# Kernel optimization log

Hardware: AMD Instinct MI355X
Metric: run time of the kernel (lower is better)

Reference implementation:

```python
import jax, jax.numpy as jnp
import numpy as np

B, C, H, W = 4, 128, 64, 64
THITA = 1e-4


def conv1x1(x, w, b):
    # 1x1 conv + bias + ReLU; x:[B,Cin,H,W], w:[Cout,Cin], b:[Cout]
    return jax.nn.relu(jnp.einsum('bihw,oi->bohw', x, w) + b[None, :, None, None])


_CONV_SPECS = [
    ('neighbor', 2 * C, 4),
    ('pro_key', C, C), ('pro_val', C, C),
    ('lat_key', C, C), ('lat_val', C, C),
    ('tmp1', C, 2 * C),
    ('now1', C, 2),
    ('now_key', C, C), ('now_val', C, C),
    ('q', C, C), ('k', C, C), ('v', C, C),
]


def setup_inputs() -> dict:
    key = jax.random.key(0)
    ks = jax.random.split(key, 1 + 2 * len(_CONV_SPECS))
    inp = {'event': jax.random.normal(ks[0], (B, 6, H, W), dtype=jnp.float32)}
    i = 1
    for name, o, c in _CONV_SPECS:
        s = 1.0 / np.sqrt(c)
        inp['w_' + name] = jax.random.uniform(ks[i], (o, c), minval=-s, maxval=s, dtype=jnp.float32)
        inp['b_' + name] = jax.random.uniform(ks[i + 1], (o,), minval=-s, maxval=s, dtype=jnp.float32)
        i += 2
    return inp


def reference(event, w_neighbor, b_neighbor, w_pro_key, b_pro_key, w_pro_val, b_pro_val,
              w_lat_key, b_lat_key, w_lat_val, b_lat_val, w_tmp1, b_tmp1,
              w_now1, b_now1, w_now_key, b_now_key, w_now_val, b_now_val,
              w_q, b_q, w_k, b_k, w_v, b_v):
    pro, now, lat = event[:, 0:2], event[:, 2:4], event[:, 4:6]
    neigh = conv1x1(jnp.concatenate([pro, lat], axis=1), w_neighbor, b_neighbor)  # [B,2C,H,W]
    pro_key = conv1x1(neigh[:, :C], w_pro_key, b_pro_key)
    pro_val = conv1x1(neigh[:, C:], w_pro_val, b_pro_val)
    lat_key = conv1x1(neigh[:, :C], w_lat_key, b_lat_key)
    lat_val = conv1x1(neigh[:, C:], w_lat_val, b_lat_val)
    # NOTE: source applies conv_tmp1 (shared weights) to both key and val paths
    key_n = conv1x1(jnp.concatenate([pro_key, lat_key], axis=1), w_tmp1, b_tmp1)
    val_n = conv1x1(jnp.concatenate([pro_val, lat_val], axis=1), w_tmp1, b_tmp1)
    now_f = conv1x1(now, w_now1, b_now1)
    now_key = conv1x1(now_f, w_now_key, b_now_key)
    now_val = conv1x1(now_f, w_now_val, b_now_val)
    N = H * W
    q = conv1x1(key_n, w_q, b_q).reshape(B, C, N)          # proj_query pre-permute
    k = conv1x1(now_key, w_k, b_k).reshape(B, C, N)        # [B,C,N]
    attn = jax.nn.softmax(jnp.einsum('bcn,bcm->bnm', q, k), axis=-1)  # [B,N,N]
    v = conv1x1(val_n, w_v, b_v).reshape(B, C, N)
    out = jnp.einsum('bcm,bnm->bcn', v, attn).reshape(B, C, H, W)
    return THITA * out + now_val
```

## Files before the change

kernel.cpp:

```cpp
#include <hip/hip_runtime.h>

#define B_ 4
#define C_ 128
#define N_ 4096
#define LOG2E 1.44269504088896340736f

typedef __attribute__((ext_vector_type(8))) __bf16 bf16x8;
typedef __attribute__((ext_vector_type(16))) float f32x16;

#define SWZ(n) (((n) & 15) << 4)

__device__ __forceinline__ unsigned short cvb(float x) {
    return __builtin_bit_cast(unsigned short, (__bf16)x);
}
__device__ __forceinline__ unsigned pk2(float lo, float hi) {
    return (unsigned)cvb(lo) | ((unsigned)cvb(hi) << 16);
}
__device__ __forceinline__ float bfu(unsigned short u) {
    return __builtin_bit_cast(float, (unsigned)u << 16);
}
__device__ __forceinline__ float fexp2(float x) {
#if __has_builtin(__builtin_amdgcn_exp2f)
    return __builtin_amdgcn_exp2f(x);
#else
    float r;
    asm("v_exp_f32 %0, %1" : "=v"(r) : "v"(x));
    return r;
#endif
}
__device__ inline void gload_lds16(const void* g, void* l) {
    __builtin_amdgcn_global_load_lds(
        (const __attribute__((address_space(1))) unsigned int*)g,
        (__attribute__((address_space(3))) unsigned int*)l, 16, 0, 0);
}
__device__ __forceinline__ void plswapf(float& a, float& b) {
    asm volatile("v_permlane32_swap_b32 %0, %1" : "+v"(a), "+v"(b));
}
__device__ __forceinline__ void plswapu(unsigned& a, unsigned& b) {
    asm volatile("v_permlane32_swap_b32 %0, %1" : "+v"(a), "+v"(b));
}

__global__ __launch_bounds__(256) void k_wcvt(
        const float* pk, const float* lk, const float* pv, const float* lv,
        const float* t1, const float* nk, const float* nv,
        const float* q, const float* k, const float* v,
        const float* bpk, const float* blk, const float* bpv, const float* blv,
        const float* bnk, const float* bnv,
        unsigned short* Wk, unsigned short* Wv, unsigned short* Wt1,
        unsigned short* Wnow, unsigned short* Wq, unsigned short* Wkk,
        unsigned short* Wvv, float* bck, float* bcv, float* bcn) {
    int i = blockIdx.x * 256 + threadIdx.x;
    if (i < 22528) {
        int c = i;
        const float *s0, *s1 = nullptr;
        unsigned short* dst;
        int ks;
        if      (c < 4096)  { dst = Wk;   ks = 3; s0 = pk; s1 = lk; }
        else if (c < 8192)  { dst = Wv;   ks = 3; s0 = pv; s1 = lv; c -= 4096; }
        else if (c < 12288) { dst = Wt1;  ks = 4; s0 = t1;          c -= 8192; }
        else if (c < 16384) { dst = Wnow; ks = 3; s0 = nk; s1 = nv; c -= 12288; }
        else if (c < 18432) { dst = Wq;   ks = 3; s0 = q;           c -= 16384; }
        else if (c < 20480) { dst = Wkk;  ks = 3; s0 = k;           c -= 18432; }
        else                { dst = Wvv;  ks = 3; s0 = v;           c -= 20480; }
        int K = 16 << ks;
        int lane = c & 63, tile = c >> 6;
        int mt = tile >> ks, kt = tile & ((1 << ks) - 1);
        int row = mt * 32 + (lane & 31);
        int col = kt * 16 + (lane >> 5) * 8;
        const float* src = (s1 && row >= 128) ? (s1 + (size_t)(row - 128) * K + col)
                                              : (s0 + (size_t)row * K + col);
        unsigned short ov[8];
        #pragma unroll
        for (int j = 0; j < 8; ++j) ov[j] = cvb(src[j]);
        *(uint4*)(dst + (size_t)c * 8) = *(const uint4*)ov;
    }
    else if (i < 22784) { int j = i - 22528; bck[j] = j < 128 ? bpk[j] : blk[j - 128]; }
    else if (i < 23040) { int j = i - 22784; bcv[j] = j < 128 ? bpv[j] : blv[j - 128]; }
    else if (i < 23296) { int j = i - 23040; bcn[j] = j < 128 ? bnk[j] : bnv[j - 128]; }
}

template<int KSTEPS, int ROWB>
__device__ __forceinline__ f32x16 gtile(const char* Ab, int aChBase,
        const unsigned short* Wf, int mchunk, int nl, int h) {
    f32x16 acc;
    #pragma unroll
    for (int r = 0; r < 16; ++r) acc[r] = 0.f;
    const char* arow = Ab + nl * ROWB;
    const unsigned short* wb = Wf + ((size_t)mchunk * KSTEPS) * 512 + (nl + 32 * h) * 8;
    #pragma unroll
    for (int kk = 0; kk < KSTEPS; ++kk) {
        bf16x8 a = *(const bf16x8*)(arow + ((aChBase + kk * 32 + h * 16) ^ SWZ(nl)));
        bf16x8 wf = *(const bf16x8*)(wb + kk * 512);
        acc = __builtin_amdgcn_mfma_f32_32x32x16_bf16(a, wf, acc, 0, 0, 0);
    }
    return acc;
}

__device__ __forceinline__ void epi_lds(char* dst, int rowB, f32x16 acc,
        const float* bias, int m0, int nl, int h) {
    int m = m0 + nl;
    float bs = bias[m];
    #pragma unroll
    for (int r = 0; r < 16; ++r) {
        int n = (r & 3) + 8 * (r >> 2) + 4 * h;
        *(unsigned short*)(dst + n * rowB + ((m * 2) ^ SWZ(n))) =
            cvb(fmaxf(acc[r] + bs, 0.f));
    }
}

__device__ __forceinline__ void epi_nc(unsigned short* Y, f32x16 acc,
        const float* bias, float scale, int m0, int n0g, int b, int nl, int h) {
    int m = m0 + nl;
    float bs = bias[m];
    #pragma unroll
    for (int r = 0; r < 16; ++r) {
        int n = (r & 3) + 8 * (r >> 2) + 4 * h;
        Y[((size_t)b * N_ + n0g + n) * C_ + m] = cvb(fmaxf(acc[r] + bs, 0.f) * scale);
    }
}

__device__ __forceinline__ void epi_cn_b16(unsigned short* Y, f32x16 acc,
        const float* bias, int m0, int n0g, int b, int nl, int h) {
    int m = m0 + nl;
    float bs = bias[m];
    #pragma unroll
    for (int r2 = 0; r2 < 4; ++r2) {
        int nn = 8 * r2 + 4 * h;
        uint2 o;
        o.x = pk2(fmaxf(acc[4*r2+0] + bs, 0.f), fmaxf(acc[4*r2+1] + bs, 0.f));
        o.y = pk2(fmaxf(acc[4*r2+2] + bs, 0.f), fmaxf(acc[4*r2+3] + bs, 0.f));
        *(uint2*)(Y + ((size_t)b * C_ + m) * N_ + n0g + nn) = o;
    }
}

__global__ __launch_bounds__(256) void k_chain(
        const float* __restrict__ ev, const float* __restrict__ w_nb,
        const float* __restrict__ b_nb, const float* __restrict__ w_n1,
        const float* __restrict__ b_n1,
        const unsigned short* __restrict__ Wk, const unsigned short* __restrict__ Wv,
        const unsigned short* __restrict__ Wt1, const unsigned short* __restrict__ Wnow,
        const unsigned short* __restrict__ Wq, const unsigned short* __restrict__ Wkk,
        const unsigned short* __restrict__ Wvv,
        const float* __restrict__ bck, const float* __restrict__ bcv,
        const float* __restrict__ bt1, const float* __restrict__ bcn,
        const float* __restrict__ bq, const float* __restrict__ bk,
        const float* __restrict__ bv,
        unsigned short* __restrict__ Qt, unsigned short* __restrict__ Kb,
        unsigned short* __restrict__ Vb, unsigned short* __restrict__ NowVb) {
    __shared__ char lds[49152];
    char* NEIGH = lds;
    char* KCAT  = lds + 16384;
    char* VCAT  = lds + 32768;
    char* KEYN  = lds;
    char* VALN  = lds + 8192;
    char* NOWF  = lds + 16384;
    char* NOWK  = lds + 24576;

    const int t = threadIdx.x, lane = t & 63, w = t >> 6;
    const int nl = lane & 31, h = lane >> 5;
    const int b = blockIdx.y;
    const int n0g = blockIdx.x * 32;
    const int m0 = w * 32;
    const int mc = w;

    uint2 nf[4];
    {
        int n = t & 31, grp = t >> 5;
        const float* evb = ev + (size_t)b * 6 * N_ + n0g + n;
        float e0 = evb[0], e1 = evb[N_], e4 = evb[4*N_], e5 = evb[5*N_];
        float e2 = evb[2*N_], e3 = evb[3*N_];
        int och0 = grp * 32;
        #pragma unroll
        for (int i = 0; i < 32; i += 4) {
            float r_[4];
            #pragma unroll
            for (int j = 0; j < 4; ++j) {
                int o = och0 + i + j;
                float4 w4 = *(const float4*)(w_nb + o * 4);
                r_[j] = fmaxf(b_nb[o] + w4.x*e0 + w4.y*e1 + w4.z*e4 + w4.w*e5, 0.f);
            }
            uint2 val; val.x = pk2(r_[0], r_[1]); val.y = pk2(r_[2], r_[3]);
            *(uint2*)(NEIGH + n * 512 + (((och0 + i) * 2) ^ SWZ(n))) = val;
        }
        int o0 = grp * 16;
        #pragma unroll
        for (int i2 = 0; i2 < 4; ++i2) {
            float r_[4];
            #pragma unroll
            for (int j = 0; j < 4; ++j) {
                int o = o0 + i2 * 4 + j;
                float2 w2 = *(const float2*)(w_n1 + o * 2);
                r_[j] = fmaxf(b_n1[o] + w2.x*e2 + w2.y*e3, 0.f);
            }
            nf[i2].x = pk2(r_[0], r_[1]); nf[i2].y = pk2(r_[2], r_[3]);
        }
    }
    __syncthreads();

    {
        f32x16 a0 = gtile<8, 512>(NEIGH, 0,   Wk, mc,     nl, h);
        f32x16 a1 = gtile<8, 512>(NEIGH, 0,   Wk, mc + 4, nl, h);
        f32x16 a2 = gtile<8, 512>(NEIGH, 256, Wv, mc,     nl, h);
        f32x16 a3 = gtile<8, 512>(NEIGH, 256, Wv, mc + 4, nl, h);
        epi_lds(KCAT, 512, a0, bck, m0,       nl, h);
        epi_lds(KCAT, 512, a1, bck, m0 + 128, nl, h);
        epi_lds(VCAT, 512, a2, bcv, m0,       nl, h);
        epi_lds(VCAT, 512, a3, bcv, m0 + 128, nl, h);
    }
    __syncthreads();

    {
        f32x16 a0 = gtile<16, 512>(KCAT, 0, Wt1, mc, nl, h);
        f32x16 a1 = gtile<16, 512>(VCAT, 0, Wt1, mc, nl, h);
        epi_lds(KEYN, 256, a0, bt1, m0, nl, h);
        epi_lds(VALN, 256, a1, bt1, m0, nl, h);
    }
    __syncthreads();

    {
        int n = t & 31, grp = t >> 5;
        int o0 = grp * 16;
        #pragma unroll
        for (int i2 = 0; i2 < 4; ++i2)
            *(uint2*)(NOWF + n * 256 + (((o0 + i2 * 4) * 2) ^ SWZ(n))) = nf[i2];
    }
    __syncthreads();

    {
        f32x16 a0 = gtile<8, 256>(NOWF, 0, Wnow, mc,     nl, h);
        f32x16 a1 = gtile<8, 256>(NOWF, 0, Wnow, mc + 4, nl, h);
        epi_lds(NOWK, 256, a0, bcn, m0, nl, h);
        epi_cn_b16(NowVb, a1, bcn + 128, m0, n0g, b, nl, h);
    }
    __syncthreads();

    {
        f32x16 aq = gtile<8, 256>(KEYN, 0, Wq,  mc, nl, h);
        f32x16 ak = gtile<8, 256>(NOWK, 0, Wkk, mc, nl, h);
        f32x16 av = gtile<8, 256>(VALN, 0, Wvv, mc, nl, h);
        epi_nc(Qt, aq, bq, LOG2E, m0, n0g, b, nl, h);
        epi_nc(Kb, ak, bk, 1.0f,  m0, n0g, b, nl, h);
        epi_cn_b16(Vb, av, bv, m0, n0g, b, nl, h);
    }
}

#define SPLIT 4
#define CHUNK 32

__global__ __launch_bounds__(128) void k_flashp(
        const unsigned short* __restrict__ Qt, const unsigned short* __restrict__ Kt,
        const unsigned short* __restrict__ Vb,
        unsigned short* __restrict__ Opb, float* __restrict__ ML) {
    __shared__ char stg[2][16384];
    const int t = threadIdx.x;
    const int lane = t & 63;
    const int nh = t >> 6;
    const int h = lane >> 5, nl = lane & 31;
    const int i_ = blockIdx.x;
    const int mpb = (i_ & 7) + 8 * ((i_ >> 3) & 1);
    const int ntile = i_ >> 4;
    const int mp = mpb >> 2, b = mpb & 3;
    const int n0 = ntile * 64 + nh * 32;
    const size_t bo = (size_t)b * N_ * C_;

    bf16x8 qf[8];
    {
        const char* qb = (const char*)(Qt + bo);
        #pragma unroll
        for (int kk = 0; kk < 8; ++kk)
            qf[kk] = *(const bf16x8*)(qb + (size_t)(n0 + nl) * 256 + kk*32 + h*16);
    }

    const char* ktb = (const char*)(Kt + bo);
    const char* vbb = (const char*)(Vb + bo);

    f32x16 oa[4];
    #pragma unroll
    for (int ss = 0; ss < 4; ++ss)
        #pragma unroll
        for (int r = 0; r < 16; ++r) oa[ss][r] = 0.f;
    float m_run = -1e30f, l_run = 0.f;

    const int swzK = (nl & 15) << 4;
    const int swzV = ((nl >> 1) & 7) << 4;

    auto stage = [&](int tile, int ph) {
        char* base = stg[ph];
        if (nh == 0) {
            const char* src = ktb + (size_t)tile * 8192;
            #pragma unroll
            for (int ii = 0; ii < 8; ++ii) {
                int L = ii*1024 + lane*16;
                int T = L ^ (((L >> 8) & 15) << 4);
                gload_lds16(src + T, base + ii*1024);
            }
        } else {
            const char* src = vbb + (size_t)tile * 64;
            #pragma unroll
            for (int ii = 0; ii < 8; ++ii) {
                int L = ii*1024 + lane*16;
                int T = L ^ (((L >> 7) & 7) << 4);
                int c = T >> 6, inner = T & 63;
                gload_lds16(src + (size_t)c * (N_*2) + inner, base + 8192 + ii*1024);
            }
        }
    };

    const int tb = mp * CHUNK;
    stage(tb, 0);
    stage(tb + 1, 1);

    for (int it = 0; it < CHUNK; ++it) {
        int ph = it & 1;
        if (it < CHUNK - 1) asm volatile("s_waitcnt vmcnt(8)" ::: "memory");
        else                asm volatile("s_waitcnt vmcnt(0)" ::: "memory");
        __builtin_amdgcn_s_barrier();
        __builtin_amdgcn_sched_barrier(0);
        const char* kb = stg[ph];
        const char* vb = kb + 8192;

        f32x16 s;
        #pragma unroll
        for (int r = 0; r < 16; ++r) s[r] = 0.f;
        __builtin_amdgcn_s_setprio(1);
        #pragma unroll
        for (int kk = 0; kk < 8; ++kk) {
            int y = nl*256 + kk*32 + h*16;
            bf16x8 a = *(const bf16x8*)(kb + (y ^ swzK));
            s = __builtin_amdgcn_mfma_f32_32x32x16_bf16(a, qf[kk], s, 0, 0, 0);
        }
        __builtin_amdgcn_s_setprio(0);

        float tm = fmaxf(fmaxf(fmaxf(s[0], s[1]), fmaxf(s[2], s[3])),
                         fmaxf(fmaxf(s[4], s[5]), fmaxf(s[6], s[7])));
        float tm2 = fmaxf(fmaxf(fmaxf(s[8], s[9]), fmaxf(s[10], s[11])),
                          fmaxf(fmaxf(s[12], s[13]), fmaxf(s[14], s[15])));
        tm = fmaxf(tm, tm2);
        { float x = tm, y = tm; plswapf(x, y); tm = fmaxf(x, y); }
        if (!__all(tm <= m_run + 8.f)) {
            float mn = fmaxf(m_run, tm);
            float sc = fexp2(m_run - mn);
            m_run = mn;
            l_run *= sc;
            #pragma unroll
            for (int ss = 0; ss < 4; ++ss)
                #pragma unroll
                for (int r = 0; r < 16; ++r) oa[ss][r] *= sc;
        }
        float p[16];
        float ls = 0.f;
        #pragma unroll
        for (int r = 0; r < 16; ++r) { p[r] = fexp2(s[r] - m_run); ls += p[r]; }
        { float x = ls, y = ls; plswapf(x, y); ls = x + y; }
        l_run += ls;

        unsigned pk_[8];
        #pragma unroll
        for (int q = 0; q < 8; ++q) pk_[q] = pk2(p[2*q], p[2*q+1]);
        unsigned a0 = pk_[0], a1 = pk_[1], b0 = pk_[2], b1 = pk_[3];
        plswapu(a0, b0); plswapu(a1, b1);
        unsigned c0 = pk_[4], c1 = pk_[5], d0 = pk_[6], d1 = pk_[7];
        plswapu(c0, d0); plswapu(c1, d1);
        typedef __attribute__((ext_vector_type(4))) unsigned u32x4;
        u32x4 uw0 = {a0, a1, b0, b1};
        u32x4 uw1 = {c0, c1, d0, d1};
        bf16x8 pf0 = __builtin_bit_cast(bf16x8, uw0);
        bf16x8 pf1 = __builtin_bit_cast(bf16x8, uw1);

        __builtin_amdgcn_s_setprio(1);
        #pragma unroll
        for (int ss = 0; ss < 4; ++ss) {
            int y0 = (32*ss + nl)*64 + h*16;
            bf16x8 va0 = *(const bf16x8*)(vb + (y0 ^ swzV));
            oa[ss] = __builtin_amdgcn_mfma_f32_32x32x16_bf16(va0, pf0, oa[ss], 0, 0, 0);
            bf16x8 va1 = *(const bf16x8*)(vb + ((y0 + 32) ^ swzV));
            oa[ss] = __builtin_amdgcn_mfma_f32_32x32x16_bf16(va1, pf1, oa[ss], 0, 0, 0);
        }
        __builtin_amdgcn_s_setprio(0);

        __builtin_amdgcn_sched_barrier(0);
        __builtin_amdgcn_s_barrier();
        if (it + 2 < CHUNK) stage(tb + it + 2, ph);
    }

    const size_t pb = (size_t)(mp * B_ + b) * 64 + ntile;
    if (h == 0) {
        ML[pb*128 +      nh*32 + nl] = m_run;
        ML[pb*128 + 64 + nh*32 + nl] = l_run;
    }
    unsigned short* dst = Opb + pb * 8192;
    #pragma unroll
    for (int ss = 0; ss < 4; ++ss)
        #pragma unroll
        for (int r = 0; r < 16; ++r) {
            int c = 32*ss + (r&3) + 8*(r>>2) + 4*h;
            dst[c*64 + nh*32 + nl] = cvb(oa[ss][r]);
        }
}

__global__ __launch_bounds__(256) void k_comb(const unsigned short* __restrict__ Opb,
        const float* __restrict__ ML, const unsigned short* __restrict__ NVb,
        float* __restrict__ out) {
    const int t = threadIdx.x;
    const int ntile = blockIdx.x, b = blockIdx.y;
    const int n = t & 63, tq = t >> 6;
    float mj[SPLIT], lj[SPLIT], wj[SPLIT];
    #pragma unroll
    for (int j = 0; j < SPLIT; ++j) {
        size_t pb = (size_t)(j * B_ + b) * 64 + ntile;
        mj[j] = ML[pb*128 + n];
        lj[j] = ML[pb*128 + 64 + n];
    }
    float M = -1e30f;
    #pragma unroll
    for (int j = 0; j < SPLIT; ++j) M = fmaxf(M, mj[j]);
    float den = 0.f;
    #pragma unroll
    for (int j = 0; j < SPLIT; ++j) { wj[j] = fexp2(mj[j] - M); den += lj[j] * wj[j]; }
    float sc = 1e-4f / den;
    #pragma unroll 4
    for (int c = tq; c < C_; c += 4) {
        float v = 0.f;
        #pragma unroll
        for (int j = 0; j < SPLIT; ++j)
            v += bfu(Opb[((size_t)(j * B_ + b) * 64 + ntile) * 8192 + c*64 + n]) * wj[j];
        size_t gi = ((size_t)b * C_ + c) * N_ + ntile*64 + n;
        out[gi] = sc * v + bfu(NVb[gi]);
    }
}

extern "C" void kernel_launch(void* const* d_in, const int* in_sizes, int n_in,
                              void* d_out, int out_size, void* d_ws, size_t ws_size,
                              hipStream_t stream) {
    const float* ev   = (const float*)d_in[0];
    const float* w_nb = (const float*)d_in[1];  const float* b_nb = (const float*)d_in[2];
    const float* w_pk = (const float*)d_in[3];  const float* b_pk = (const float*)d_in[4];
    const float* w_pv = (const float*)d_in[5];  const float* b_pv = (const float*)d_in[6];
    const float* w_lk = (const float*)d_in[7];  const float* b_lk = (const float*)d_in[8];
    const float* w_lv = (const float*)d_in[9];  const float* b_lv = (const float*)d_in[10];
    const float* w_t1 = (const float*)d_in[11]; const float* b_t1 = (const float*)d_in[12];
    const float* w_n1 = (const float*)d_in[13]; const float* b_n1 = (const float*)d_in[14];
    const float* w_nk = (const float*)d_in[15]; const float* b_nk = (const float*)d_in[16];
    const float* w_nv = (const float*)d_in[17]; const float* b_nv = (const float*)d_in[18];
    const float* w_q  = (const float*)d_in[19]; const float* b_q  = (const float*)d_in[20];
    const float* w_k  = (const float*)d_in[21]; const float* b_k  = (const float*)d_in[22];
    const float* w_v  = (const float*)d_in[23]; const float* b_v  = (const float*)d_in[24];

    char* p = (char*)d_ws;
    unsigned short* Qt = (unsigned short*)p; p += (size_t)B_*N_*C_*2;
    unsigned short* Kb = (unsigned short*)p; p += (size_t)B_*N_*C_*2;
    unsigned short* Vb = (unsigned short*)p; p += (size_t)B_*C_*N_*2;
    unsigned short* NowVb = (unsigned short*)p; p += (size_t)B_*C_*N_*2;
    unsigned short* Wk   = (unsigned short*)p; p += 32768*2;
    unsigned short* Wv   = (unsigned short*)p; p += 32768*2;
    unsigned short* Wt1  = (unsigned short*)p; p += 32768*2;
    unsigned short* Wnow = (unsigned short*)p; p += 32768*2;
    unsigned short* Wq   = (unsigned short*)p; p += 16384*2;
    unsigned short* Wkk  = (unsigned short*)p; p += 16384*2;
    unsigned short* Wvv  = (unsigned short*)p; p += 16384*2;
    float* bck = (float*)p; p += 256*4;
    float* bcv = (float*)p; p += 256*4;
    float* bcn = (float*)p; p += 256*4;
    p = (char*)(((size_t)p + 255) & ~(size_t)255);
    unsigned short* Opb = (unsigned short*)p; p += (size_t)SPLIT*B_*64*8192*2;
    float* ML = (float*)p; p += (size_t)SPLIT*B_*64*128*4;

    k_wcvt<<<dim3(91), dim3(256), 0, stream>>>(
        w_pk, w_lk, w_pv, w_lv, w_t1, w_nk, w_nv, w_q, w_k, w_v,
        b_pk, b_lk, b_pv, b_lv, b_nk, b_nv,
        Wk, Wv, Wt1, Wnow, Wq, Wkk, Wvv, bck, bcv, bcn);

    k_chain<<<dim3(N_/32, B_), dim3(256), 0, stream>>>(
        ev, w_nb, b_nb, w_n1, b_n1,
        Wk, Wv, Wt1, Wnow, Wq, Wkk, Wvv,
        bck, bcv, b_t1, bcn, b_q, b_k, b_v,
        Qt, Kb, Vb, NowVb);

    k_flashp<<<dim3(N_/64 * SPLIT * B_), dim3(128), 0, stream>>>(Qt, Kb, Vb, Opb, ML);

    k_comb<<<dim3(N_/64, B_), dim3(256), 0, stream>>>(Opb, ML, NowVb, (float*)d_out);
}
```

Baseline: 84.74 us.

## Software-pipeline QK^T of next tile with softmax of current in flash kernel

Splits the shared staging buffer into separate K and V double buffers. K tiles are now prefetched at the top of each iteration and V tiles at the bottom. The QK^T MFMAs for tile it+1 are issued before the softmax and PV work of tile it, so matrix work can overlap the exp and reduction math. This holds an extra f32x16 score accumulator live per lane, adds register pressure, and needs a prologue barrier.

```diff
diff --git a/kernel.cpp b/kernel.cpp
--- a/kernel.cpp
+++ b/kernel.cpp
@@ -251,7 +251,8 @@
         const unsigned short* __restrict__ Qt, const unsigned short* __restrict__ Kt,
         const unsigned short* __restrict__ Vb,
         unsigned short* __restrict__ Opb, float* __restrict__ ML) {
-    __shared__ char stg[2][16384];
+    __shared__ char stgK[2][8192];
+    __shared__ char stgV[2][8192];
     const int t = threadIdx.x;
     const int lane = t & 63;
     const int nh = t >> 6;
@@ -284,52 +285,69 @@
     const int swzK = (nl & 15) << 4;
     const int swzV = ((nl >> 1) & 7) << 4;
 
-    auto stage = [&](int tile, int ph) {
-        char* base = stg[ph];
-        if (nh == 0) {
-            const char* src = ktb + (size_t)tile * 8192;
-            #pragma unroll
-            for (int ii = 0; ii < 8; ++ii) {
-                int L = ii*1024 + lane*16;
-                int T = L ^ (((L >> 8) & 15) << 4);
-                gload_lds16(src + T, base + ii*1024);
-            }
-        } else {
-            const char* src = vbb + (size_t)tile * 64;
-            #pragma unroll
-            for (int ii = 0; ii < 8; ++ii) {
-                int L = ii*1024 + lane*16;
-                int T = L ^ (((L >> 7) & 7) << 4);
-                int c = T >> 6, inner = T & 63;
-                gload_lds16(src + (size_t)c * (N_*2) + inner, base + 8192 + ii*1024);
-            }
+    auto stageK = [&](int tile, int ph) {
+        const char* src = ktb + (size_t)tile * 8192;
+        char* base = stgK[ph];
+        #pragma unroll
+        for (int ii = 0; ii < 8; ++ii) {
+            int L = ii*1024 + lane*16;
+            int T = L ^ (((L >> 8) & 15) << 4);
+            gload_lds16(src + T, base + ii*1024);
         }
     };
-
-    const int tb = mp * CHUNK;
-    stage(tb, 0);
-    stage(tb + 1, 1);
-
-    for (int it = 0; it < CHUNK; ++it) {
-        int ph = it & 1;
-        if (it < CHUNK - 1) asm volatile("s_waitcnt vmcnt(8)" ::: "memory");
-        else                asm volatile("s_waitcnt vmcnt(0)" ::: "memory");
-        __builtin_amdgcn_s_barrier();
-        __builtin_amdgcn_sched_barrier(0);
-        const char* kb = stg[ph];
-        const char* vb = kb + 8192;
-
+    auto stageV = [&](int tile, int ph) {
+        const char* src = vbb + (size_t)tile * 64;
+        char* base = stgV[ph];
+        #pragma unroll
+        for (int ii = 0; ii < 8; ++ii) {
+            int L = ii*1024 + lane*16;
+            int T = L ^ (((L >> 7) & 7) << 4);
+            int c = T >> 6, inner = T & 63;
+            gload_lds16(src + (size_t)c * (N_*2) + inner, base + ii*1024);
+        }
+    };
+
+    auto qk_tile = [&](const char* kb) {
         f32x16 s;
         #pragma unroll
         for (int r = 0; r < 16; ++r) s[r] = 0.f;
-        __builtin_amdgcn_s_setprio(1);
         #pragma unroll
         for (int kk = 0; kk < 8; ++kk) {
             int y = nl*256 + kk*32 + h*16;
             bf16x8 a = *(const bf16x8*)(kb + (y ^ swzK));
             s = __builtin_amdgcn_mfma_f32_32x32x16_bf16(a, qf[kk], s, 0, 0, 0);
         }
-        __builtin_amdgcn_s_setprio(0);
+        return s;
+    };
+
+    const int tb = mp * CHUNK;
+    if (nh == 0) { stageK(tb, 0); stageK(tb + 1, 1); }
+    else         { stageV(tb, 0); stageV(tb + 1, 1); }
+    asm volatile("s_waitcnt vmcnt(0)" ::: "memory");
+    __builtin_amdgcn_s_barrier();
+    __builtin_amdgcn_sched_barrier(0);
+
+    f32x16 s = qk_tile(stgK[0]);
+    __builtin_amdgcn_sched_barrier(0);
+    __builtin_amdgcn_s_barrier();
+
+    for (int it = 0; it < CHUNK; ++it) {
+        const int ph = it & 1;
+        if (it + 2 < CHUNK) {
+            if (nh == 0) stageK(tb + it + 2, ph);
+            asm volatile("s_waitcnt vmcnt(8)" ::: "memory");
+        } else {
+            asm volatile("s_waitcnt vmcnt(0)" ::: "memory");
+        }
+        __builtin_amdgcn_s_barrier();
+        __builtin_amdgcn_sched_barrier(0);
+
+        f32x16 s_next;
+        if (it + 1 < CHUNK) {
+            __builtin_amdgcn_s_setprio(1);
+            s_next = qk_tile(stgK[(it + 1) & 1]);
+            __builtin_amdgcn_s_setprio(0);
+        }
 
         float tm = fmaxf(fmaxf(fmaxf(s[0], s[1]), fmaxf(s[2], s[3])),
                          fmaxf(fmaxf(s[4], s[5]), fmaxf(s[6], s[7])));
@@ -367,6 +385,7 @@
         bf16x8 pf0 = __builtin_bit_cast(bf16x8, uw0);
         bf16x8 pf1 = __builtin_bit_cast(bf16x8, uw1);
 
+        const char* vb = stgV[ph];
         __builtin_amdgcn_s_setprio(1);
         #pragma unroll
         for (int ss = 0; ss < 4; ++ss) {
@@ -380,7 +399,8 @@
 
         __builtin_amdgcn_sched_barrier(0);
         __builtin_amdgcn_s_barrier();
-        if (it + 2 < CHUNK) stage(tb + it + 2, ph);
+        if (it + 2 < CHUNK && nh == 1) stageV(tb + it + 2, ph);
+        if (it + 1 < CHUNK) s = s_next;
     }
 
     const size_t pb = (size_t)(mp * B_ + b) * 64 + ntile;
```

Result: no change. 86.10 us (+1.6%).

## Fuse split-K combine into flash kernel via last-block atomic counter

Applied to the files above, without the earlier changes.

Removes the separate combine kernel. Each flash block increments a per-(batch, tile) atomic counter after writing its partial output, and the last of the SPLIT blocks merges the partials with the now_val residual. The counters are zeroed in the weight-conversion kernel. This saves one kernel launch and its tail, at the cost of thread fences, an atomic per block, and a serialized combine done by 128 threads instead of 256 in the last block.

```diff
diff --git a/kernel.cpp b/kernel.cpp
--- a/kernel.cpp
+++ b/kernel.cpp
@@ -48,7 +48,7 @@
         const float* bnk, const float* bnv,
         unsigned short* Wk, unsigned short* Wv, unsigned short* Wt1,
         unsigned short* Wnow, unsigned short* Wq, unsigned short* Wkk,
-        unsigned short* Wvv, float* bck, float* bcv, float* bcn) {
+        unsigned short* Wvv, float* bck, float* bcv, float* bcn, int* cnt) {
     int i = blockIdx.x * 256 + threadIdx.x;
     if (i < 22528) {
         int c = i;
@@ -77,6 +77,7 @@
     else if (i < 22784) { int j = i - 22528; bck[j] = j < 128 ? bpk[j] : blk[j - 128]; }
     else if (i < 23040) { int j = i - 22784; bcv[j] = j < 128 ? bpv[j] : blv[j - 128]; }
     else if (i < 23296) { int j = i - 23040; bcn[j] = j < 128 ? bnk[j] : bnv[j - 128]; }
+    else if (i < 23552) { cnt[i - 23296] = 0; }
 }
 
 template<int KSTEPS, int ROWB>
@@ -250,8 +251,11 @@
 __global__ __launch_bounds__(128) void k_flashp(
         const unsigned short* __restrict__ Qt, const unsigned short* __restrict__ Kt,
         const unsigned short* __restrict__ Vb,
-        unsigned short* __restrict__ Opb, float* __restrict__ ML) {
+        unsigned short* __restrict__ Opb, float* __restrict__ ML,
+        const unsigned short* __restrict__ NVb, float* __restrict__ out,
+        int* __restrict__ cnt) {
     __shared__ char stg[2][16384];
+    __shared__ int lastflag;
     const int t = threadIdx.x;
     const int lane = t & 63;
     const int nh = t >> 6;
@@ -396,20 +400,24 @@
             int c = 32*ss + (r&3) + 8*(r>>2) + 4*h;
             dst[c*64 + nh*32 + nl] = cvb(oa[ss][r]);
         }
-}
-
-__global__ __launch_bounds__(256) void k_comb(const unsigned short* __restrict__ Opb,
-        const float* __restrict__ ML, const unsigned short* __restrict__ NVb,
-        float* __restrict__ out) {
-    const int t = threadIdx.x;
-    const int ntile = blockIdx.x, b = blockIdx.y;
-    const int n = t & 63, tq = t >> 6;
+
+    __threadfence();
+    __syncthreads();
+    if (t == 0) {
+        int prev = atomicAdd(&cnt[b * 64 + ntile], 1);
+        lastflag = (prev == SPLIT - 1);
+    }
+    __syncthreads();
+    if (!lastflag) return;
+    __threadfence();
+
+    const int n2 = t & 63, cq = t >> 6;
     float mj[SPLIT], lj[SPLIT], wj[SPLIT];
     #pragma unroll
     for (int j = 0; j < SPLIT; ++j) {
-        size_t pb = (size_t)(j * B_ + b) * 64 + ntile;
-        mj[j] = ML[pb*128 + n];
-        lj[j] = ML[pb*128 + 64 + n];
+        size_t pbj = (size_t)(j * B_ + b) * 64 + ntile;
+        mj[j] = ML[pbj*128 + n2];
+        lj[j] = ML[pbj*128 + 64 + n2];
     }
     float M = -1e30f;
     #pragma unroll
@@ -417,15 +425,14 @@
     float den = 0.f;
     #pragma unroll
     for (int j = 0; j < SPLIT; ++j) { wj[j] = fexp2(mj[j] - M); den += lj[j] * wj[j]; }
-    float sc = 1e-4f / den;
-    #pragma unroll 4
-    for (int c = tq; c < C_; c += 4) {
+    float scl = 1e-4f / den;
+    for (int c = cq; c < C_; c += 2) {
         float v = 0.f;
         #pragma unroll
         for (int j = 0; j < SPLIT; ++j)
-            v += bfu(Opb[((size_t)(j * B_ + b) * 64 + ntile) * 8192 + c*64 + n]) * wj[j];
-        size_t gi = ((size_t)b * C_ + c) * N_ + ntile*64 + n;
-        out[gi] = sc * v + bfu(NVb[gi]);
+            v += bfu(Opb[((size_t)(j * B_ + b) * 64 + ntile) * 8192 + c*64 + n2]) * wj[j];
+        size_t gi = ((size_t)b * C_ + c) * N_ + ntile*64 + n2;
+        out[gi] = scl * v + bfu(NVb[gi]);
     }
 }
 
@@ -464,11 +471,12 @@
     p = (char*)(((size_t)p + 255) & ~(size_t)255);
     unsigned short* Opb = (unsigned short*)p; p += (size_t)SPLIT*B_*64*8192*2;
     float* ML = (float*)p; p += (size_t)SPLIT*B_*64*128*4;
-
-    k_wcvt<<<dim3(91), dim3(256), 0, stream>>>(
+    int* cnt = (int*)p; p += 256*4;
+
+    k_wcvt<<<dim3(92), dim3(256), 0, stream>>>(
         w_pk, w_lk, w_pv, w_lv, w_t1, w_nk, w_nv, w_q, w_k, w_v,
         b_pk, b_lk, b_pv, b_lv, b_nk, b_nv,
-        Wk, Wv, Wt1, Wnow, Wq, Wkk, Wvv, bck, bcv, bcn);
+        Wk, Wv, Wt1, Wnow, Wq, Wkk, Wvv, bck, bcv, bcn, cnt);
 
     k_chain<<<dim3(N_/32, B_), dim3(256), 0, stream>>>(
         ev, w_nb, b_nb, w_n1, b_n1,
@@ -476,7 +484,6 @@
         bck, bcv, b_t1, bcn, b_q, b_k, b_v,
         Qt, Kb, Vb, NowVb);
 
-    k_flashp<<<dim3(N_/64 * SPLIT * B_), dim3(128), 0, stream>>>(Qt, Kb, Vb, Opb, ML);
-
-    k_comb<<<dim3(N_/64, B_), dim3(256), 0, stream>>>(Opb, ML, NowVb, (float*)d_out);
-}
+    k_flashp<<<dim3(N_/64 * SPLIT * B_), dim3(128), 0, stream>>>(
+        Qt, Kb, Vb, Opb, ML, NowVb, (float*)d_out, cnt);
+}
```

New measurement: 179.1 us. 2.11x slower.
